# Optimization experiments

Hardware: AMD Instinct MI355X
Metric: run time of the kernel (lower is better)

The kernel has to match this reference:

```python
import jax, jax.numpy as jnp
import numpy as np

D_MODEL = 1024
NUM_HEADS = 16
D_K = D_MODEL // NUM_HEADS


def setup_inputs() -> dict:
    key = jax.random.key(0)
    ks = jax.random.split(key, 10)
    s = 1.0 / np.sqrt(D_MODEL)  # ~ torch Linear init scale
    inp = {
        "x": jax.random.normal(ks[0], (2, 2048, D_MODEL), dtype=jnp.float32),
        "Wq": jax.random.uniform(ks[1], (D_MODEL, D_MODEL), jnp.float32, -s, s),
        "bq": jax.random.uniform(ks[2], (D_MODEL,), jnp.float32, -s, s),
        "Wk": jax.random.uniform(ks[3], (D_MODEL, D_MODEL), jnp.float32, -s, s),
        "bk": jax.random.uniform(ks[4], (D_MODEL,), jnp.float32, -s, s),
        "Wv": jax.random.uniform(ks[5], (D_MODEL, D_MODEL), jnp.float32, -s, s),
        "bv": jax.random.uniform(ks[6], (D_MODEL,), jnp.float32, -s, s),
        "Wo": jax.random.uniform(ks[7], (D_MODEL, D_MODEL), jnp.float32, -s, s),
        "bo": jax.random.uniform(ks[8], (D_MODEL,), jnp.float32, -s, s),
        "ln_gamma": jnp.ones((D_MODEL,), jnp.float32),
        "ln_beta": jnp.zeros((D_MODEL,), jnp.float32),
    }
    return inp


def reference(x, Wq, bq, Wk, bk, Wv, bv, Wo, bo, ln_gamma, ln_beta):
    B, S, D = x.shape
    residual = x
    # LayerNorm (eps=1e-5 as torch default)
    mu = jnp.mean(x, axis=-1, keepdims=True)
    var = jnp.mean(jnp.square(x - mu), axis=-1, keepdims=True)
    xn = (x - mu) * jax.lax.rsqrt(var + 1e-5) * ln_gamma + ln_beta
    # QKV projections (torch Linear: y = x @ W^T + b) -> (B, H, S, d_k)
    def proj(W, b):
        return (xn @ W.T + b).reshape(B, S, NUM_HEADS, D_K).transpose(0, 2, 1, 3)
    Q, K, V = proj(Wq, bq), proj(Wk, bk), proj(Wv, bv)
    scores = jnp.einsum("bhqd,bhkd->bhqk", Q, K) / np.sqrt(D_K).astype(np.float32)
    attn = jax.nn.softmax(scores, axis=-1)  # (B, H, S, S); dropout is no-op (eval)
    context = jnp.einsum("bhqk,bhkd->bhqd", attn, V)
    context = context.transpose(0, 2, 1, 3).reshape(B, S, D)
    out = context @ Wo.T + bo
    return out + residual, attn.mean(axis=1)
```

## Files before the change

### kernel.cpp

```cpp
#include <hip/hip_runtime.h>
#include <stdint.h>
#include <stddef.h>

#define DEV static __device__ __forceinline__

typedef float f32x4 __attribute__((ext_vector_type(4)));
typedef float f32x16 __attribute__((ext_vector_type(16)));
typedef unsigned u32x4 __attribute__((ext_vector_type(4)));
typedef __bf16 bf16x8 __attribute__((ext_vector_type(8)));

DEV short f2bf(float f) {
  union { float f; unsigned u; } a; a.f = f;
  unsigned r = a.u + 0x7fffu + ((a.u >> 16) & 1u);
  return (short)(r >> 16);
}

DEV void gld_lds16(const void* g, void* lds) {
  __builtin_amdgcn_global_load_lds(
      (__attribute__((address_space(1))) void*)(void*)g,
      (__attribute__((address_space(3))) void*)lds, 16, 0, 0);
}

DEV f32x4 MFMA(bf16x8 a, bf16x8 b, f32x4 c) {
  return __builtin_amdgcn_mfma_f32_16x16x32_bf16(a, b, c, 0, 0, 0);
}
DEV f32x16 MFMA32(bf16x8 a, bf16x8 b, f32x16 c) {
  return __builtin_amdgcn_mfma_f32_32x32x16_bf16(a, b, c, 0, 0, 0);
}

DEV float ex2(float x) { return __builtin_amdgcn_exp2f(x); }

DEV unsigned cvtpk(float lo, float hi) {
  unsigned r;
  asm("v_cvt_pk_bf16_f32 %0, %1, %2" : "=v"(r) : "v"(lo), "v"(hi));
  return r;
}

DEV float xhalf_max(float v) {
  float a = v, b = v;
  asm volatile("v_permlane32_swap_b32 %0, %1" : "+v"(a), "+v"(b));
  return fmaxf(a, b);
}
DEV float xhalf_sum(float v) {
  float a = v, b = v;
  asm volatile("v_permlane32_swap_b32 %0, %1" : "+v"(a), "+v"(b));
  return a + b;
}

#define LOG2E 1.4426950408889634f


__global__ __launch_bounds__(256) void k_cvtw(const float* __restrict__ w0,
                                              const float* __restrict__ w1,
                                              const float* __restrict__ w2,
                                              const float* __restrict__ w3,
                                              short* __restrict__ dst) {
  int i = blockIdx.x * 256 + threadIdx.x;
  int sel = i >> 18;
  const float* src = sel == 0 ? w0 : sel == 1 ? w1 : sel == 2 ? w2 : w3;
  int off = (i & 0x3ffff) * 4;
  float4 v = *(const float4*)(src + off);
  short4 o4; o4.x = f2bf(v.x); o4.y = f2bf(v.y); o4.z = f2bf(v.z); o4.w = f2bf(v.w);
  *(short4*)(dst + (size_t)i * 4) = o4;
}

__global__ __launch_bounds__(256) void k_ln(const float* __restrict__ x,
                                            const float* __restrict__ g,
                                            const float* __restrict__ be,
                                            short* __restrict__ xn) {
  int row = blockIdx.x;
  int t = threadIdx.x;
  const float4* xr = (const float4*)(x + (size_t)row * 1024);
  float4 v = xr[t];
  float s = v.x + v.y + v.z + v.w;
  float ss = v.x * v.x + v.y * v.y + v.z * v.z + v.w * v.w;
#pragma unroll
  for (int o = 32; o; o >>= 1) { s += __shfl_down(s, o); ss += __shfl_down(ss, o); }
  __shared__ float ps[4], pss[4];
  int w = t >> 6, lane = t & 63;
  if (lane == 0) { ps[w] = s; pss[w] = ss; }
  __syncthreads();
  float st = ps[0] + ps[1] + ps[2] + ps[3];
  float sst = pss[0] + pss[1] + pss[2] + pss[3];
  float mean = st * (1.0f / 1024.0f);
  float var = sst * (1.0f / 1024.0f) - mean * mean;
  float rstd = rsqrtf(var + 1e-5f);
  float4 gv = ((const float4*)g)[t];
  float4 bv = ((const float4*)be)[t];
  short4 o4;
  o4.x = f2bf((v.x - mean) * rstd * gv.x + bv.x);
  o4.y = f2bf((v.y - mean) * rstd * gv.y + bv.y);
  o4.z = f2bf((v.z - mean) * rstd * gv.z + bv.z);
  o4.w = f2bf((v.w - mean) * rstd * gv.w + bv.w);
  ((short4*)(xn + (size_t)row * 1024))[t] = o4;
}

__global__ __launch_bounds__(256) void k_gemm_qkv(
    const short* __restrict__ xn, const short* __restrict__ wbf,
    const float* __restrict__ bq, const float* __restrict__ bk,
    const float* __restrict__ bv, short* __restrict__ q_ws,
    short* __restrict__ k_ws, short* __restrict__ v_ws) {
  __shared__ __align__(16) short at[128 * 32];
  __shared__ __align__(16) short bt[128 * 32];
  int t = threadIdx.x, lane = t & 63, w = t >> 6;
  int wr = w >> 1, wc = w & 1;
  int z = blockIdx.z;
  int row0 = blockIdx.y * 128, col0 = blockIdx.x * 128;
  const short* A = xn + (size_t)row0 * 1024;
  const short* Bw = wbf + (size_t)z * (1024 * 1024) + (size_t)col0 * 1024;
  f32x4 acc[4][4];
#pragma unroll
  for (int m = 0; m < 4; m++)
#pragma unroll
    for (int n = 0; n < 4; n++) acc[m][n] = (f32x4)0.0f;

  for (int k0 = 0; k0 < 1024; k0 += 32) {
#pragma unroll
    for (int i = 0; i < 2; i++) {
      int c = t + i * 256;
      int r = c >> 2, cc = (c & 3) * 8;
      gld_lds16(A + (size_t)r * 1024 + k0 + cc, &at[c * 8]);
      gld_lds16(Bw + (size_t)r * 1024 + k0 + cc, &bt[c * 8]);
    }
    __syncthreads();
    bf16x8 af[4], bfr[4];
#pragma unroll
    for (int m = 0; m < 4; m++)
      af[m] = *(const bf16x8*)&at[(wr * 64 + m * 16 + (lane & 15)) * 32 + (lane >> 4) * 8];
#pragma unroll
    for (int n = 0; n < 4; n++)
      bfr[n] = *(const bf16x8*)&bt[(wc * 64 + n * 16 + (lane & 15)) * 32 + (lane >> 4) * 8];
#pragma unroll
    for (int m = 0; m < 4; m++)
#pragma unroll
      for (int n = 0; n < 4; n++) acc[m][n] = MFMA(af[m], bfr[n], acc[m][n]);
    __syncthreads();
  }
  const float* bias = z == 0 ? bq : z == 1 ? bk : bv;
  short* dst = z == 0 ? q_ws : z == 1 ? k_ws : v_ws;
  float scal = z == 0 ? (0.125f * LOG2E) : 1.0f;
#pragma unroll
  for (int m = 0; m < 4; m++)
#pragma unroll
    for (int n = 0; n < 4; n++)
#pragma unroll
      for (int r = 0; r < 4; r++) {
        int grow = row0 + wr * 64 + m * 16 + (lane >> 4) * 4 + r;
        int gcol = col0 + wc * 64 + n * 16 + (lane & 15);
        float val = (acc[m][n][r] + bias[gcol]) * scal;
        int bb = grow >> 11, s = grow & 2047, h = gcol >> 6, d = gcol & 63;
        dst[(((size_t)bb * 16 + h) * 2048 + s) * 64 + d] = f2bf(val);
      }
}

__global__ __launch_bounds__(256) void k_trv(const short* __restrict__ v_ws,
                                             short* __restrict__ vt_ws) {
  __shared__ short tile[64][65];
  int bh = blockIdx.y, s0 = blockIdx.x * 64;
  const short* src = v_ws + ((size_t)bh * 2048 + s0) * 64;
  int t = threadIdx.x;
#pragma unroll
  for (int i = 0; i < 4; i++) {
    int c = t + i * 256;
    int r = c >> 4, d4 = (c & 15) * 4;
    short4 v4 = *(const short4*)&src[r * 64 + d4];
    tile[d4 + 0][r] = v4.x; tile[d4 + 1][r] = v4.y;
    tile[d4 + 2][r] = v4.z; tile[d4 + 3][r] = v4.w;
  }
  __syncthreads();
#pragma unroll
  for (int i = 0; i < 4; i++) {
    int c = t + i * 256;
    int d = c >> 4, r4 = (c & 15) * 4;
    short4 o4;
    o4.x = tile[d][r4 + 0]; o4.y = tile[d][r4 + 1];
    o4.z = tile[d][r4 + 2]; o4.w = tile[d][r4 + 3];
    *(short4*)&vt_ws[((size_t)bh * 64 + d) * 2048 + s0 + r4] = o4;
  }
}

__global__ __launch_bounds__(256) void k_attn1(
    const short* __restrict__ q_ws, const short* __restrict__ k_ws,
    const short* __restrict__ vt_ws, short* __restrict__ o_ws,
    float* __restrict__ m_ws, float* __restrict__ l_ws) {
  __shared__ __align__(16) short k_lds[2][64 * 64];
  __shared__ __align__(16) short vt_lds[2][64 * 64];
  int t = threadIdx.x, lane = t & 63, w = t >> 6;
  int hi = lane >> 5, l31 = lane & 31;
  int qt = blockIdx.x, hd = blockIdx.y, b = blockIdx.z;
  int bh = b * 16 + hd;
  int q0 = qt * 128;
  const short* qb = q_ws + (size_t)bh * (2048 * 64);
  const short* kb = k_ws + (size_t)bh * (2048 * 64);
  const short* vtb = vt_ws + (size_t)bh * (64 * 2048);
  int qg = q0 + w * 32 + l31;

  bf16x8 qf[4];
#pragma unroll
  for (int d4 = 0; d4 < 4; d4++)
    qf[d4] = *(const bf16x8*)&qb[(size_t)qg * 64 + d4 * 16 + hi * 8];
  asm volatile("s_waitcnt vmcnt(0)" ::: "memory");

  const short *kp0, *kp1, *vp0, *vp1;
  {
    int c = t, r = c >> 3, j = (c & 7) ^ (r & 7);
    kp0 = kb + (size_t)r * 64 + j * 8;
    vp0 = vtb + (size_t)r * 2048 + j * 8;
  }
  {
    int c = t + 256, r = c >> 3, j = (c & 7) ^ (r & 7);
    kp1 = kb + (size_t)r * 64 + j * 8;
    vp1 = vtb + (size_t)r * 2048 + j * 8;
  }

#define STG_K(kt_, buf)                                     \
  {                                                         \
    gld_lds16(kp0 + (kt_) * 4096, &k_lds[buf][t * 8]);      \
    gld_lds16(kp1 + (kt_) * 4096, &k_lds[buf][(t + 256) * 8]); \
  }
#define STG_V(kt_, buf)                                     \
  {                                                         \
    gld_lds16(vp0 + (kt_) * 64, &vt_lds[buf][t * 8]);       \
    gld_lds16(vp1 + (kt_) * 64, &vt_lds[buf][(t + 256) * 8]); \
  }

  STG_K(0, 0);

  f32x16 Oacc[2];
#pragma unroll
  for (int i = 0; i < 16; i++) { Oacc[0][i] = 0.0f; Oacc[1][i] = 0.0f; }
  float mrun = -1e30f, lrun = 0.0f;
  bf16x8 pb0, pb1, pb2, pb3;

  for (int it = 0; it < 32; ++it) {
    STG_V(it, it & 1);
    STG_K(it < 31 ? it + 1 : 31, (it + 1) & 1);
    asm volatile("s_waitcnt vmcnt(4)" ::: "memory");
    __builtin_amdgcn_s_barrier();

    const short* kl = k_lds[it & 1];
    const short* vl = vt_lds[(it ^ 1) & 1];

    __builtin_amdgcn_s_setprio(1);
    f32x16 S0 = (f32x16)0.0f, S1 = (f32x16)0.0f;
#pragma unroll
    for (int d4 = 0; d4 < 4; d4++) {
      int row0 = l31;
      bf16x8 kf0 = *(const bf16x8*)&kl[row0 * 64 + (((d4 * 2 + hi) ^ (row0 & 7)) * 8)];
      int row1 = 32 + l31;
      bf16x8 kf1 = *(const bf16x8*)&kl[row1 * 64 + (((d4 * 2 + hi) ^ (row1 & 7)) * 8)];
      S0 = MFMA32(kf0, qf[d4], S0);
      S1 = MFMA32(kf1, qf[d4], S1);
    }
    if (it) {
#pragma unroll
      for (int ks = 0; ks < 4; ks++) {
        bf16x8 pk = ks == 0 ? pb0 : ks == 1 ? pb1 : ks == 2 ? pb2 : pb3;
        int row0 = l31;
        bf16x8 vf0 = *(const bf16x8*)&vl[row0 * 64 + (((ks * 2 + hi) ^ (row0 & 7)) * 8)];
        int row1 = 32 + l31;
        bf16x8 vf1 = *(const bf16x8*)&vl[row1 * 64 + (((ks * 2 + hi) ^ (row1 & 7)) * 8)];
        Oacc[0] = MFMA32(vf0, pk, Oacc[0]);
        Oacc[1] = MFMA32(vf1, pk, Oacc[1]);
      }
    }
    __builtin_amdgcn_s_setprio(0);

    float mt;
    {
      float a[8];
#pragma unroll
      for (int i = 0; i < 8; i++)
        a[i] = fmaxf(fmaxf(S0[i], S0[i + 8]), fmaxf(S1[i], S1[i + 8]));
      float b0 = fmaxf(fmaxf(a[0], a[1]), fmaxf(a[2], a[3]));
      float b1 = fmaxf(fmaxf(a[4], a[5]), fmaxf(a[6], a[7]));
      mt = xhalf_max(fmaxf(b0, b1));
    }
    if (!__all(mt - mrun <= 8.0f)) {
      float mn = fmaxf(mrun, mt);
      float sc_ = ex2(mrun - mn);
      lrun *= sc_;
#pragma unroll
      for (int i = 0; i < 16; i++) { Oacc[0][i] *= sc_; Oacc[1][i] *= sc_; }
      mrun = mn;
    }
    float rs0 = 0.0f, rs1 = 0.0f;
#pragma unroll
    for (int i = 0; i < 16; i++) {
      float p0 = ex2(S0[i] - mrun);
      float p1 = ex2(S1[i] - mrun);
      S0[i] = p0; S1[i] = p1;
      rs0 += p0; rs1 += p1;
    }
    lrun += xhalf_sum(rs0 + rs1);

    {
      unsigned wA, wB, wC, wD;
      wA = cvtpk(S0[0], S0[1]);  wB = cvtpk(S0[2], S0[3]);
      wC = cvtpk(S0[4], S0[5]);  wD = cvtpk(S0[6], S0[7]);
      asm volatile("v_permlane32_swap_b32 %0, %1" : "+v"(wA), "+v"(wC));
      asm volatile("v_permlane32_swap_b32 %0, %1" : "+v"(wB), "+v"(wD));
      u32x4 uu; uu.x = wA; uu.y = wB; uu.z = wC; uu.w = wD;
      pb0 = __builtin_bit_cast(bf16x8, uu);
      wA = cvtpk(S0[8], S0[9]);  wB = cvtpk(S0[10], S0[11]);
      wC = cvtpk(S0[12], S0[13]); wD = cvtpk(S0[14], S0[15]);
      asm volatile("v_permlane32_swap_b32 %0, %1" : "+v"(wA), "+v"(wC));
      asm volatile("v_permlane32_swap_b32 %0, %1" : "+v"(wB), "+v"(wD));
      uu.x = wA; uu.y = wB; uu.z = wC; uu.w = wD;
      pb1 = __builtin_bit_cast(bf16x8, uu);
      wA = cvtpk(S1[0], S1[1]);  wB = cvtpk(S1[2], S1[3]);
      wC = cvtpk(S1[4], S1[5]);  wD = cvtpk(S1[6], S1[7]);
      asm volatile("v_permlane32_swap_b32 %0, %1" : "+v"(wA), "+v"(wC));
      asm volatile("v_permlane32_swap_b32 %0, %1" : "+v"(wB), "+v"(wD));
      uu.x = wA; uu.y = wB; uu.z = wC; uu.w = wD;
      pb2 = __builtin_bit_cast(bf16x8, uu);
      wA = cvtpk(S1[8], S1[9]);  wB = cvtpk(S1[10], S1[11]);
      wC = cvtpk(S1[12], S1[13]); wD = cvtpk(S1[14], S1[15]);
      asm volatile("v_permlane32_swap_b32 %0, %1" : "+v"(wA), "+v"(wC));
      asm volatile("v_permlane32_swap_b32 %0, %1" : "+v"(wB), "+v"(wD));
      uu.x = wA; uu.y = wB; uu.z = wC; uu.w = wD;
      pb3 = __builtin_bit_cast(bf16x8, uu);
    }
    __builtin_amdgcn_s_barrier();
  }
  asm volatile("s_waitcnt vmcnt(0)" ::: "memory");
  __builtin_amdgcn_s_barrier();

  {
    const short* vl = vt_lds[1];
    __builtin_amdgcn_s_setprio(1);
#pragma unroll
    for (int ks = 0; ks < 4; ks++) {
      bf16x8 pk = ks == 0 ? pb0 : ks == 1 ? pb1 : ks == 2 ? pb2 : pb3;
      int row0 = l31;
      bf16x8 vf0 = *(const bf16x8*)&vl[row0 * 64 + (((ks * 2 + hi) ^ (row0 & 7)) * 8)];
      int row1 = 32 + l31;
      bf16x8 vf1 = *(const bf16x8*)&vl[row1 * 64 + (((ks * 2 + hi) ^ (row1 & 7)) * 8)];
      Oacc[0] = MFMA32(vf0, pk, Oacc[0]);
      Oacc[1] = MFMA32(vf1, pk, Oacc[1]);
    }
    __builtin_amdgcn_s_setprio(0);
  }

  float rl = 1.0f / lrun;
  if (lane < 32) {
    m_ws[bh * 2048 + qg] = mrun;
    l_ws[bh * 2048 + qg] = rl;
  }
#pragma unroll
  for (int dt = 0; dt < 2; dt++)
#pragma unroll
    for (int g = 0; g < 4; g++) {
      short4 o4;
      o4.x = f2bf(Oacc[dt][g * 4 + 0] * rl);
      o4.y = f2bf(Oacc[dt][g * 4 + 1] * rl);
      o4.z = f2bf(Oacc[dt][g * 4 + 2] * rl);
      o4.w = f2bf(Oacc[dt][g * 4 + 3] * rl);
      int d = dt * 32 + g * 8 + hi * 4;
      *(short4*)&o_ws[((size_t)(b * 2048 + qg)) * 1024 + hd * 64 + d] = o4;
    }
}

__global__ __launch_bounds__(256, 3) void k_attn2(
    const short* __restrict__ q_ws, const short* __restrict__ k_ws,
    const float* __restrict__ m_ws, const float* __restrict__ l_ws,
    float* __restrict__ out1) {
  __shared__ __align__(16) short q_lds[2][64 * 64];
  __shared__ __align__(16) short k_lds2[2][128 * 64];
  __shared__ __align__(16) float ml_lds[2][2][64];
  int t = threadIdx.x, lane = t & 63, w = t >> 6;
  int k2 = blockIdx.x * 128, q0 = blockIdx.y * 64, b = blockIdx.z;

  f32x4 pacc[8];
#pragma unroll
  for (int n = 0; n < 8; n++) pacc[n] = (f32x4)0.0f;

#define STAGE2(hh, buf)                                                          \
  {                                                                              \
    int bh_ = b * 16 + (hh);                                                     \
    const short* qb_ = q_ws + (size_t)bh_ * (2048 * 64);                         \
    const short* kb_ = k_ws + (size_t)bh_ * (2048 * 64);                         \
    _Pragma("unroll")                                                            \
    for (int i = 0; i < 2; i++) {                                                \
      int c = t + i * 256;                                                       \
      int r = c >> 3, j = (c & 7) ^ (r & 7);                                     \
      gld_lds16(qb_ + (size_t)(q0 + r) * 64 + j * 8, &q_lds[buf][c * 8]);        \
    }                                                                            \
    _Pragma("unroll")                                                            \
    for (int i = 0; i < 4; i++) {                                                \
      int c = t + i * 256;                                                       \
      int r = c >> 3, j = (c & 7) ^ (r & 7);                                     \
      gld_lds16(kb_ + (size_t)(k2 + r) * 64 + j * 8, &k_lds2[buf][c * 8]);       \
    }                                                                            \
    int cc = w * 8 + (t & 63);                                                   \
    if ((t & 63) < 8) {                                                          \
      const float* src_ = cc < 16 ? &m_ws[(size_t)bh_ * 2048 + q0 + cc * 4]      \
                                  : &l_ws[(size_t)bh_ * 2048 + q0 + (cc - 16) * 4]; \
      gld_lds16(src_, &ml_lds[buf][0][cc * 4]);                                  \
    }                                                                            \
  }

  STAGE2(0, 0);
  int cur = 0;
  for (int h = 0; h < 16; ++h) {
    int hn = h < 15 ? h + 1 : 15;
    STAGE2(hn, cur ^ 1);
    asm volatile("s_waitcnt vmcnt(7)" ::: "memory");
    __builtin_amdgcn_s_barrier();

    const short* ql = q_lds[cur];
    const short* kl = k_lds2[cur];
    bf16x8 qf[2];
#pragma unroll
    for (int kf = 0; kf < 2; kf++) {
      int row = w * 16 + (lane & 15);
      qf[kf] = *(const bf16x8*)&ql[row * 64 + (((kf * 4 + (lane >> 4)) ^ (row & 7)) * 8)];
    }
    f32x4 sc[8];
#pragma unroll
    for (int n = 0; n < 8; n++) sc[n] = (f32x4)0.0f;
#pragma unroll
    for (int kf = 0; kf < 2; kf++)
#pragma unroll
      for (int n = 0; n < 8; n++) {
        int row = n * 16 + (lane & 15);
        bf16x8 kfr = *(const bf16x8*)&kl[row * 64 + (((kf * 4 + (lane >> 4)) ^ (row & 7)) * 8)];
        sc[n] = MFMA(qf[kf], kfr, sc[n]);
      }
    f32x4 mh = *(const f32x4*)&ml_lds[cur][0][w * 16 + (lane >> 4) * 4];
    f32x4 lh = *(const f32x4*)&ml_lds[cur][1][w * 16 + (lane >> 4) * 4];
#pragma unroll
    for (int n = 0; n < 8; n++)
#pragma unroll
      for (int r = 0; r < 4; r++)
        pacc[n][r] += ex2(sc[n][r] - mh[r]) * lh[r];
    __builtin_amdgcn_s_barrier();
    cur ^= 1;
  }

#pragma unroll
  for (int n = 0; n < 8; n++)
#pragma unroll
    for (int r = 0; r < 4; r++) {
      int q = q0 + w * 16 + (lane >> 4) * 4 + r;
      int k = k2 + n * 16 + (lane & 15);
      out1[((size_t)b * 2048 + q) * 2048 + k] = pacc[n][r] * 0.0625f;
    }
}

__global__ __launch_bounds__(256) void k_gemm_out(
    const short* __restrict__ o_ws, const short* __restrict__ wo_bf,
    const float* __restrict__ bo, const float* __restrict__ x,
    float* __restrict__ out0) {
  __shared__ __align__(16) short at[128 * 32];
  __shared__ __align__(16) short bt[128 * 32];
  int t = threadIdx.x, lane = t & 63, w = t >> 6;
  int wr = w >> 1, wc = w & 1;
  int row0 = blockIdx.y * 128, col0 = blockIdx.x * 128;
  const short* A = o_ws + (size_t)row0 * 1024;
  const short* Bw = wo_bf + (size_t)col0 * 1024;
  f32x4 acc[4][4];
#pragma unroll
  for (int m = 0; m < 4; m++)
#pragma unroll
    for (int n = 0; n < 4; n++) acc[m][n] = (f32x4)0.0f;

  for (int k0 = 0; k0 < 1024; k0 += 32) {
#pragma unroll
    for (int i = 0; i < 2; i++) {
      int c = t + i * 256;
      int r = c >> 2, cc = (c & 3) * 8;
      gld_lds16(A + (size_t)r * 1024 + k0 + cc, &at[c * 8]);
      gld_lds16(Bw + (size_t)r * 1024 + k0 + cc, &bt[c * 8]);
    }
    __syncthreads();
    bf16x8 af[4], bfr[4];
#pragma unroll
    for (int m = 0; m < 4; m++)
      af[m] = *(const bf16x8*)&at[(wr * 64 + m * 16 + (lane & 15)) * 32 + (lane >> 4) * 8];
#pragma unroll
    for (int n = 0; n < 4; n++)
      bfr[n] = *(const bf16x8*)&bt[(wc * 64 + n * 16 + (lane & 15)) * 32 + (lane >> 4) * 8];
#pragma unroll
    for (int m = 0; m < 4; m++)
#pragma unroll
      for (int n = 0; n < 4; n++) acc[m][n] = MFMA(af[m], bfr[n], acc[m][n]);
    __syncthreads();
  }
#pragma unroll
  for (int m = 0; m < 4; m++)
#pragma unroll
    for (int n = 0; n < 4; n++)
#pragma unroll
      for (int r = 0; r < 4; r++) {
        int grow = row0 + wr * 64 + m * 16 + (lane >> 4) * 4 + r;
        int gcol = col0 + wc * 64 + n * 16 + (lane & 15);
        float val = acc[m][n][r] + bo[gcol] + x[(size_t)grow * 1024 + gcol];
        out0[(size_t)grow * 1024 + gcol] = val;
      }
}

extern "C" void kernel_launch(void* const* d_in, const int* in_sizes, int n_in,
                              void* d_out, int out_size, void* d_ws, size_t ws_size,
                              hipStream_t stream) {
  (void)in_sizes; (void)n_in; (void)out_size; (void)ws_size;
  const float* x   = (const float*)d_in[0];
  const float* Wq  = (const float*)d_in[1];
  const float* bq  = (const float*)d_in[2];
  const float* Wk  = (const float*)d_in[3];
  const float* bk  = (const float*)d_in[4];
  const float* Wv  = (const float*)d_in[5];
  const float* bv  = (const float*)d_in[6];
  const float* Wo  = (const float*)d_in[7];
  const float* bo  = (const float*)d_in[8];
  const float* lng = (const float*)d_in[9];
  const float* lnb = (const float*)d_in[10];
  float* out0 = (float*)d_out;
  float* out1 = out0 + (size_t)2 * 2048 * 1024;

  char* ws = (char*)d_ws;
  short* xn    = (short*)(ws);
  short* q_ws  = (short*)(ws + 8388608);
  short* k_ws  = (short*)(ws + 16777216);
  short* o_ws  = (short*)(ws + 25165824);
  short* vt_ws = (short*)(ws + 33554432);
  short* wbf   = (short*)(ws + 41943040);
  float* m_ws  = (float*)(ws + 50331648);
  float* l_ws  = (float*)(ws + 50593792);

  k_cvtw<<<4096, 256, 0, stream>>>(Wq, Wk, Wv, Wo, wbf);
  k_ln<<<4096, 256, 0, stream>>>(x, lng, lnb, xn);
  k_gemm_qkv<<<dim3(8, 32, 3), 256, 0, stream>>>(xn, wbf, bq, bk, bv, q_ws, k_ws, o_ws);
  k_trv<<<dim3(32, 32), 256, 0, stream>>>(o_ws, vt_ws);
  k_attn1<<<dim3(16, 16, 2), 256, 0, stream>>>(q_ws, k_ws, vt_ws, o_ws, m_ws, l_ws);
  k_attn2<<<dim3(16, 32, 2), 256, 0, stream>>>(q_ws, k_ws, m_ws, l_ws, out1);
  k_gemm_out<<<dim3(8, 32), 256, 0, stream>>>(o_ws, wbf + (size_t)3 * 1024 * 1024, bo, x, out0);
}
```

Before: 168.1 us.

## Merge weight-convert and LayerNorm kernels; deepen attention K/V prefetch to four buffers

Combines the bf16 weight conversion and LayerNorm into one launch split by block index, removing a kernel launch and its serialization gap. In the first attention kernel, K and V^T tiles now go through a 4-deep LDS ring, prefetched two iterations ahead, instead of a 2-deep ring with K and V staggered. This gives global-to-LDS loads more time to land before each barrier, but doubles LDS use per block, which may reduce occupancy.

```diff
diff --git a/kernel.cpp b/kernel.cpp
--- a/kernel.cpp
+++ b/kernel.cpp
@@ -4,6 +4,7 @@
 
 #define DEV static __device__ __forceinline__
 
+typedef float f32x2 __attribute__((ext_vector_type(2)));
 typedef float f32x4 __attribute__((ext_vector_type(4)));
 typedef float f32x16 __attribute__((ext_vector_type(16)));
 typedef unsigned u32x4 __attribute__((ext_vector_type(4)));
@@ -50,49 +51,47 @@
 #define LOG2E 1.4426950408889634f
 
 
-__global__ __launch_bounds__(256) void k_cvtw(const float* __restrict__ w0,
-                                              const float* __restrict__ w1,
-                                              const float* __restrict__ w2,
-                                              const float* __restrict__ w3,
-                                              short* __restrict__ dst) {
-  int i = blockIdx.x * 256 + threadIdx.x;
-  int sel = i >> 18;
-  const float* src = sel == 0 ? w0 : sel == 1 ? w1 : sel == 2 ? w2 : w3;
-  int off = (i & 0x3ffff) * 4;
-  float4 v = *(const float4*)(src + off);
-  short4 o4; o4.x = f2bf(v.x); o4.y = f2bf(v.y); o4.z = f2bf(v.z); o4.w = f2bf(v.w);
-  *(short4*)(dst + (size_t)i * 4) = o4;
-}
-
-__global__ __launch_bounds__(256) void k_ln(const float* __restrict__ x,
-                                            const float* __restrict__ g,
-                                            const float* __restrict__ be,
-                                            short* __restrict__ xn) {
-  int row = blockIdx.x;
-  int t = threadIdx.x;
-  const float4* xr = (const float4*)(x + (size_t)row * 1024);
-  float4 v = xr[t];
-  float s = v.x + v.y + v.z + v.w;
-  float ss = v.x * v.x + v.y * v.y + v.z * v.z + v.w * v.w;
-#pragma unroll
-  for (int o = 32; o; o >>= 1) { s += __shfl_down(s, o); ss += __shfl_down(ss, o); }
+__global__ __launch_bounds__(256) void k_cvtw_ln(
+    const float* __restrict__ w0, const float* __restrict__ w1,
+    const float* __restrict__ w2, const float* __restrict__ w3,
+    short* __restrict__ dst, const float* __restrict__ x,
+    const float* __restrict__ g, const float* __restrict__ be,
+    short* __restrict__ xn) {
   __shared__ float ps[4], pss[4];
-  int w = t >> 6, lane = t & 63;
-  if (lane == 0) { ps[w] = s; pss[w] = ss; }
-  __syncthreads();
-  float st = ps[0] + ps[1] + ps[2] + ps[3];
-  float sst = pss[0] + pss[1] + pss[2] + pss[3];
-  float mean = st * (1.0f / 1024.0f);
-  float var = sst * (1.0f / 1024.0f) - mean * mean;
-  float rstd = rsqrtf(var + 1e-5f);
-  float4 gv = ((const float4*)g)[t];
-  float4 bv = ((const float4*)be)[t];
-  short4 o4;
-  o4.x = f2bf((v.x - mean) * rstd * gv.x + bv.x);
-  o4.y = f2bf((v.y - mean) * rstd * gv.y + bv.y);
-  o4.z = f2bf((v.z - mean) * rstd * gv.z + bv.z);
-  o4.w = f2bf((v.w - mean) * rstd * gv.w + bv.w);
-  ((short4*)(xn + (size_t)row * 1024))[t] = o4;
+  if (blockIdx.x < 4096) {
+    int i = blockIdx.x * 256 + threadIdx.x;
+    int sel = i >> 18;
+    const float* src = sel == 0 ? w0 : sel == 1 ? w1 : sel == 2 ? w2 : w3;
+    int off = (i & 0x3ffff) * 4;
+    float4 v = *(const float4*)(src + off);
+    short4 o4; o4.x = f2bf(v.x); o4.y = f2bf(v.y); o4.z = f2bf(v.z); o4.w = f2bf(v.w);
+    *(short4*)(dst + (size_t)i * 4) = o4;
+  } else {
+    int row = blockIdx.x - 4096;
+    int t = threadIdx.x;
+    const float4* xr = (const float4*)(x + (size_t)row * 1024);
+    float4 v = xr[t];
+    float s = v.x + v.y + v.z + v.w;
+    float ss = v.x * v.x + v.y * v.y + v.z * v.z + v.w * v.w;
+#pragma unroll
+    for (int o = 32; o; o >>= 1) { s += __shfl_down(s, o); ss += __shfl_down(ss, o); }
+    int w = t >> 6, lane = t & 63;
+    if (lane == 0) { ps[w] = s; pss[w] = ss; }
+    __syncthreads();
+    float st = ps[0] + ps[1] + ps[2] + ps[3];
+    float sst = pss[0] + pss[1] + pss[2] + pss[3];
+    float mean = st * (1.0f / 1024.0f);
+    float var = sst * (1.0f / 1024.0f) - mean * mean;
+    float rstd = rsqrtf(var + 1e-5f);
+    float4 gv = ((const float4*)g)[t];
+    float4 bv = ((const float4*)be)[t];
+    short4 o4;
+    o4.x = f2bf((v.x - mean) * rstd * gv.x + bv.x);
+    o4.y = f2bf((v.y - mean) * rstd * gv.y + bv.y);
+    o4.z = f2bf((v.z - mean) * rstd * gv.z + bv.z);
+    o4.w = f2bf((v.w - mean) * rstd * gv.w + bv.w);
+    ((short4*)(xn + (size_t)row * 1024))[t] = o4;
+  }
 }
 
 __global__ __launch_bounds__(256) void k_gemm_qkv(
@@ -183,8 +182,8 @@
     const short* __restrict__ q_ws, const short* __restrict__ k_ws,
     const short* __restrict__ vt_ws, short* __restrict__ o_ws,
     float* __restrict__ m_ws, float* __restrict__ l_ws) {
-  __shared__ __align__(16) short k_lds[2][64 * 64];
-  __shared__ __align__(16) short vt_lds[2][64 * 64];
+  __shared__ __align__(16) short k_lds[4][64 * 64];
+  __shared__ __align__(16) short vt_lds[4][64 * 64];
   int t = threadIdx.x, lane = t & 63, w = t >> 6;
   int hi = lane >> 5, l31 = lane & 31;
   int qt = blockIdx.x, hd = blockIdx.y, b = blockIdx.z;
@@ -213,18 +212,16 @@
     vp1 = vtb + (size_t)r * 2048 + j * 8;
   }
 
-#define STG_K(kt_, buf)                                     \
-  {                                                         \
-    gld_lds16(kp0 + (kt_) * 4096, &k_lds[buf][t * 8]);      \
-    gld_lds16(kp1 + (kt_) * 4096, &k_lds[buf][(t + 256) * 8]); \
-  }
-#define STG_V(kt_, buf)                                     \
-  {                                                         \
-    gld_lds16(vp0 + (kt_) * 64, &vt_lds[buf][t * 8]);       \
-    gld_lds16(vp1 + (kt_) * 64, &vt_lds[buf][(t + 256) * 8]); \
-  }
-
-  STG_K(0, 0);
+#define STG(tl_, buf)                                            \
+  {                                                              \
+    gld_lds16(kp0 + (size_t)(tl_) * 4096, &k_lds[buf][t * 8]);   \
+    gld_lds16(kp1 + (size_t)(tl_) * 4096, &k_lds[buf][(t + 256) * 8]); \
+    gld_lds16(vp0 + (size_t)(tl_) * 64, &vt_lds[buf][t * 8]);    \
+    gld_lds16(vp1 + (size_t)(tl_) * 64, &vt_lds[buf][(t + 256) * 8]); \
+  }
+
+  STG(0, 0);
+  STG(1, 1);
 
   f32x16 Oacc[2];
 #pragma unroll
@@ -233,13 +230,13 @@
   bf16x8 pb0, pb1, pb2, pb3;
 
   for (int it = 0; it < 32; ++it) {
-    STG_V(it, it & 1);
-    STG_K(it < 31 ? it + 1 : 31, (it + 1) & 1);
-    asm volatile("s_waitcnt vmcnt(4)" ::: "memory");
+    int tn = it + 2 <= 31 ? it + 2 : 31;
+    STG(tn, (it + 2) & 3);
+    asm volatile("s_waitcnt vmcnt(8)" ::: "memory");
     __builtin_amdgcn_s_barrier();
 
-    const short* kl = k_lds[it & 1];
-    const short* vl = vt_lds[(it ^ 1) & 1];
+    const short* kl = k_lds[it & 3];
+    const short* vl = vt_lds[(it + 3) & 3];
 
     __builtin_amdgcn_s_setprio(1);
     f32x16 S0 = (f32x16)0.0f, S1 = (f32x16)0.0f;
@@ -327,7 +324,7 @@
   __builtin_amdgcn_s_barrier();
 
   {
-    const short* vl = vt_lds[1];
+    const short* vl = vt_lds[3];
     __builtin_amdgcn_s_setprio(1);
 #pragma unroll
     for (int ks = 0; ks < 4; ks++) {
@@ -528,8 +525,7 @@
   float* m_ws  = (float*)(ws + 50331648);
   float* l_ws  = (float*)(ws + 50593792);
 
-  k_cvtw<<<4096, 256, 0, stream>>>(Wq, Wk, Wv, Wo, wbf);
-  k_ln<<<4096, 256, 0, stream>>>(x, lng, lnb, xn);
+  k_cvtw_ln<<<8192, 256, 0, stream>>>(Wq, Wk, Wv, Wo, wbf, x, lng, lnb, xn);
   k_gemm_qkv<<<dim3(8, 32, 3), 256, 0, stream>>>(xn, wbf, bq, bk, bv, q_ws, k_ws, o_ws);
   k_trv<<<dim3(32, 32), 256, 0, stream>>>(o_ws, vt_ws);
   k_attn1<<<dim3(16, 16, 2), 256, 0, stream>>>(q_ws, k_ws, vt_ws, o_ws, m_ws, l_ws);
```

Result: no change. 167.8 us (-0.2%).
